# Kernel tuning notes

Hardware: AMD Instinct MI355X
Metric: run time of the kernel (lower is better)

## Reference

```python
import jax, jax.numpy as jnp
import numpy as np

IMG = 1024.0          # image height == width
OUT = 7               # roi_size
RATIO = 2             # sampling_ratio
SCALE = 1.0 / 32.0    # spatial_scale
BBOX_W = (10.0, 10.0, 5.0, 5.0)
DWH_CLIP = float(np.log(1000.0 / 16.0))


def _bilinear(feat, ys, xs):
    """feat [C,H,W]; ys [N,P,1], xs [N,1,P] -> [C,N,P,P] (torchvision semantics)."""
    C, H, W = feat.shape
    valid = (ys > -1.0) & (ys < H) & (xs > -1.0) & (xs < W)
    y = jnp.clip(ys, 0.0, H - 1.0)
    x = jnp.clip(xs, 0.0, W - 1.0)
    y0 = jnp.floor(y).astype(jnp.int32)
    x0 = jnp.floor(x).astype(jnp.int32)
    y1 = jnp.minimum(y0 + 1, H - 1)
    x1 = jnp.minimum(x0 + 1, W - 1)
    ly = y - y0
    lx = x - x0
    hy = 1.0 - ly
    hx = 1.0 - lx
    v = (feat[:, y0, x0] * (hy * hx) + feat[:, y0, x1] * (hy * lx)
         + feat[:, y1, x0] * (ly * hx) + feat[:, y1, x1] * (ly * lx))
    return jnp.where(valid, v, 0.0)


def _roi_align_image(feat, rois):
    """feat [C,H,W], rois [N,4] xyxy in image coords -> [N,C,OUT,OUT]."""
    b = rois * SCALE
    x1, y1 = b[:, 0], b[:, 1]
    rw = jnp.maximum(b[:, 2] - x1, 1.0)
    rh = jnp.maximum(b[:, 3] - y1, 1.0)
    bw = rw / OUT
    bh = rh / OUT
    # sub-bin sample offsets: [OUT*RATIO] positions along each roi edge
    g = (jnp.arange(OUT, dtype=jnp.float32)[:, None]
         + (jnp.arange(RATIO, dtype=jnp.float32)[None, :] + 0.5) / RATIO).reshape(-1)
    ys = y1[:, None] + g[None, :] * bh[:, None]   # [N, OUT*RATIO]
    xs = x1[:, None] + g[None, :] * bw[:, None]
    v = _bilinear(feat, ys[:, :, None], xs[:, None, :])          # [C,N,P,P]
    C = feat.shape[0]
    v = v.reshape(C, -1, OUT, RATIO, OUT, RATIO).mean(axis=(3, 5))  # avg over samples
    return jnp.transpose(v, (1, 0, 2, 3))


def _decode(deltas, proposals):
    """deltas [R,K*4], proposals [R,4] -> clipped boxes [R,K,4]."""
    wx, wy, ww, wh = BBOX_W
    pw = proposals[:, 2] - proposals[:, 0]
    ph = proposals[:, 3] - proposals[:, 1]
    cx = proposals[:, 0] + 0.5 * pw
    cy = proposals[:, 1] + 0.5 * ph
    d = deltas.reshape(deltas.shape[0], -1, 4)
    dx = d[..., 0] / wx
    dy = d[..., 1] / wy
    dw = jnp.minimum(d[..., 2] / ww, DWH_CLIP)
    dh = jnp.minimum(d[..., 3] / wh, DWH_CLIP)
    pcx = dx * pw[:, None] + cx[:, None]
    pcy = dy * ph[:, None] + cy[:, None]
    ppw = jnp.exp(dw) * pw[:, None]
    pph = jnp.exp(dh) * ph[:, None]
    boxes = jnp.stack([pcx - 0.5 * ppw, pcy - 0.5 * pph,
                       pcx + 0.5 * ppw, pcy + 0.5 * pph], axis=-1)
    return jnp.clip(boxes, 0.0, IMG)  # clip_boxes_to_image


def setup_inputs() -> dict:
    key = jax.random.key(0)
    ks = jax.random.split(key, 8)
    B, N, C, H, W = 2, 1024, 256, 32, 32
    feat_dim = C * OUT * OUT  # 12544
    features = jax.random.normal(ks[0], (B, C, H, W), dtype=jnp.float32)
    cxy = jax.random.uniform(ks[1], (B, N, 2), minval=0.0, maxval=IMG)
    wh = jax.random.uniform(ks[2], (B, N, 2), minval=16.0, maxval=256.0)
    p1 = jnp.clip(cxy - 0.5 * wh, 0.0, IMG)
    p2 = jnp.clip(cxy + 0.5 * wh, 0.0, IMG)
    proposals = jnp.concatenate([p1, p2], axis=-1)  # [B,N,4] valid xyxy
    w1 = jax.random.normal(ks[3], (1024, feat_dim), dtype=jnp.float32) * 0.01
    w2 = jax.random.normal(ks[4], (1024, 1024), dtype=jnp.float32) * 0.01
    wc = jax.random.normal(ks[5], (2, 1024), dtype=jnp.float32) * 0.01
    wb = jax.random.normal(ks[6], (8, 1024), dtype=jnp.float32) * 0.001
    return {"features": features, "proposals": proposals,
            "w1": w1, "b1": jnp.zeros((1024,), jnp.float32),
            "w2": w2, "b2": jnp.zeros((1024,), jnp.float32),
            "wc": wc, "bc": jnp.zeros((2,), jnp.float32),
            "wb": wb, "bb": jnp.zeros((8,), jnp.float32)}


def reference(features, proposals, w1, b1, w2, b2, wc, bc, wb, bb):
    pooled = jax.vmap(_roi_align_image)(features, proposals)   # [B,N,C,7,7]
    B, N = pooled.shape[:2]
    x = pooled.reshape(B * N, -1)                               # flatten(start_dim=1)
    x = jax.nn.relu(x @ w1.T + b1)
    x = jax.nn.relu(x @ w2.T + b2)
    cls_scores = x @ wc.T + bc                                  # [R, num_classes]
    bbox_deltas = x @ wb.T + bb                                 # [R, num_classes*4]
    pred_boxes = _decode(bbox_deltas, proposals.reshape(-1, 4)) # [R, num_classes, 4]
    pred_scores = jax.nn.softmax(cls_scores, axis=-1)
    return cls_scores, bbox_deltas, pred_boxes, pred_scores
```

## Files before the change

kernel.cpp:

```cpp
#include <hip/hip_runtime.h>
#include <hip/hip_bf16.h>
#include <stdint.h>

typedef __attribute__((ext_vector_type(8))) short bf16x8;
typedef __attribute__((ext_vector_type(4))) float f32x4;

__device__ __forceinline__ ushort f2bf(float f) {
    union { float f; uint32_t u; } c; c.f = f;
    uint32_t u = c.u;
    uint32_t r = (u + 0x7FFFu + ((u >> 16) & 1u)) >> 16;
    return (ushort)r;
}

__device__ __forceinline__ void load16_to_lds(const void* gsrc, void* ldst) {
    __builtin_amdgcn_global_load_lds(
        (const __attribute__((address_space(1))) uint32_t*)gsrc,
        (__attribute__((address_space(3))) uint32_t*)ldst,
        16, 0, 0);
}

__global__ __launch_bounds__(256) void f32_to_bf16_kernel(
    const float* __restrict__ in, ushort* __restrict__ out, int n)
{
    int i = (blockIdx.x * 256 + threadIdx.x) * 4;
    if (i >= n) return;
    float4 v = *(const float4*)(in + i);
    ushort4 o;
    o.x = f2bf(v.x); o.y = f2bf(v.y); o.z = f2bf(v.z); o.w = f2bf(v.w);
    *(ushort4*)(out + i) = o;
}

__global__ __launch_bounds__(256) void transpose_feat_kernel(
    const float* __restrict__ feat, float* __restrict__ featT)
{
    int bc = blockIdx.x;
    int b = bc >> 8;
    int c = bc & 255;
    const float* src = feat + (size_t)bc * 1024;
    float* dst = featT + (size_t)b * 262144 + c;
    #pragma unroll
    for (int i = 0; i < 4; ++i) {
        int p = i * 256 + threadIdx.x;
        dst[(size_t)p * 256] = src[p];
    }
}

__global__ __launch_bounds__(512) void roi_align_kernel(
    const float* __restrict__ featT, const float* __restrict__ props,
    ushort* __restrict__ pooled)
{
    int roi = blockIdx.x;
    int b = roi >> 10;
    __shared__ int   si0[28];
    __shared__ int   si1[28];
    __shared__ float sl[28];
    __shared__ float sv[28];
    __shared__ float Aw[7][10];
    __shared__ float Bw[7][10];
    __shared__ __align__(16) ushort outbuf[12544];
    int tid = threadIdx.x;
    if (tid < 28) {
        int axis = (tid >= 14) ? 1 : 0;
        int pp = tid - axis * 14;
        float c0 = props[roi * 4 + (axis ? 0 : 1)] * (1.f / 32.f);
        float c1 = props[roi * 4 + (axis ? 2 : 3)] * (1.f / 32.f);
        float sz = fmaxf(c1 - c0, 1.f);
        float bsz = sz * (1.f / 7.f);
        float g = (float)(pp >> 1) + ((float)(pp & 1) + 0.5f) * 0.5f;
        float c = c0 + g * bsz;
        float valid = (c > -1.f && c < 32.f) ? 1.f : 0.f;
        float cc = fminf(fmaxf(c, 0.f), 31.f);
        float fl = floorf(cc);
        int i0 = (int)fl;
        si0[tid] = i0;
        si1[tid] = min(i0 + 1, 31);
        sl[tid] = cc - fl;
        sv[tid] = valid;
    }
    __syncthreads();

    const int r0 = si0[0];
    const int c0 = si0[14];

    if (tid < 140) {
        int axis = tid / 70;
        int e = tid - axis * 70;
        int oy = e / 10, yy = e - oy * 10;
        int base = axis * 14;
        int org = axis ? c0 : r0;
        float wsum = 0.f;
        #pragma unroll
        for (int s = 0; s < 2; ++s) {
            int p = base + oy * 2 + s;
            float w = 0.f;
            if (si0[p] - org == yy) w += 1.f - sl[p];
            if (si1[p] - org == yy) w += sl[p];
            wsum += sv[p] * w;
        }
        wsum *= 0.5f;
        if (axis == 0) Aw[oy][yy] = wsum;
        else           Bw[oy][yy] = wsum;
    }
    __syncthreads();

    const int grp = tid >> 8;
    const int ch = tid & 255;
    const float* fbase = featT + (size_t)b * 262144 + ch;

    int xoff[10];
    #pragma unroll
    for (int x = 0; x < 10; ++x) xoff[x] = min(c0 + x, 31) * 256;

    if (grp == 0) {
        float t[4][10];
        #pragma unroll
        for (int oy = 0; oy < 4; ++oy)
            #pragma unroll
            for (int x = 0; x < 10; ++x) t[oy][x] = 0.f;
        #pragma unroll
        for (int y = 0; y < 10; ++y) {
            const float* frow = fbase + (size_t)min(r0 + y, 31) * 8192;
            float a0 = Aw[0][y], a1 = Aw[1][y], a2 = Aw[2][y], a3 = Aw[3][y];
            #pragma unroll
            for (int x = 0; x < 10; ++x) {
                float fv = frow[xoff[x]];
                t[0][x] += a0 * fv;
                t[1][x] += a1 * fv;
                t[2][x] += a2 * fv;
                t[3][x] += a3 * fv;
            }
        }
        #pragma unroll
        for (int oy = 0; oy < 4; ++oy)
            #pragma unroll
            for (int ox = 0; ox < 7; ++ox) {
                float o = 0.f;
                #pragma unroll
                for (int x = 0; x < 10; ++x) o += Bw[ox][x] * t[oy][x];
                outbuf[ch * 49 + oy * 7 + ox] = f2bf(o);
            }
    } else {
        float t[3][10];
        #pragma unroll
        for (int oy = 0; oy < 3; ++oy)
            #pragma unroll
            for (int x = 0; x < 10; ++x) t[oy][x] = 0.f;
        #pragma unroll
        for (int y = 0; y < 10; ++y) {
            const float* frow = fbase + (size_t)min(r0 + y, 31) * 8192;
            float a4 = Aw[4][y], a5 = Aw[5][y], a6 = Aw[6][y];
            #pragma unroll
            for (int x = 0; x < 10; ++x) {
                float fv = frow[xoff[x]];
                t[0][x] += a4 * fv;
                t[1][x] += a5 * fv;
                t[2][x] += a6 * fv;
            }
        }
        #pragma unroll
        for (int oy = 0; oy < 3; ++oy)
            #pragma unroll
            for (int ox = 0; ox < 7; ++ox) {
                float o = 0.f;
                #pragma unroll
                for (int x = 0; x < 10; ++x) o += Bw[ox][x] * t[oy][x];
                outbuf[ch * 49 + (4 + oy) * 7 + ox] = f2bf(o);
            }
    }
    __syncthreads();

    const uint4* src = (const uint4*)outbuf;
    uint4* dst = (uint4*)(pooled + (size_t)roi * 12544);
    #pragma unroll
    for (int i = 0; i < 4; ++i) {
        int idx = i * 512 + tid;
        if (idx < 1568) dst[idx] = src[idx];
    }
}

__global__ __launch_bounds__(256, 3) void gemm_bt_split(
    const ushort* __restrict__ A, const ushort* __restrict__ Bm,
    float* __restrict__ part, int M, int N, int K, int klen)
{
    constexpr int BK = 32;
    __shared__ __align__(16) ushort lA[128][BK];
    __shared__ __align__(16) ushort lB[128][BK];
    const int tid = threadIdx.x;

    const int nbx = gridDim.x, nby = gridDim.y;
    const int nwg = nbx * nby * gridDim.z;
    const int d = blockIdx.x + nbx * (blockIdx.y + nby * blockIdx.z);
    const int t = (d & 7) * (nwg >> 3) + (d >> 3);
    const int n_blk = t % nbx;
    const int m_blk = (t / nbx) % nby;
    const int k_blk = t / (nbx * nby);

    const int m0 = m_blk * 128;
    const int n0 = n_blk * 128;
    const int k_start = k_blk * klen;

    const int w = tid >> 6, l = tid & 63;
    const int wr = w >> 1, wcid = w & 1;
    const int lrow = l & 15;
    const int lkb = (((l >> 4) ^ ((lrow >> 1) & 3)) * 16);

    int sc0 = tid, sc1 = 256 + tid;
    int srow0 = sc0 >> 2, srow1 = sc1 >> 2;
    int scol0 = ((sc0 & 3) ^ ((srow0 >> 1) & 3)) * 16;
    int scol1 = ((sc1 & 3) ^ ((srow1 >> 1) & 3)) * 16;

    f32x4 acc[4][4] = {};

    for (int k0 = k_start; k0 < k_start + klen; k0 += BK) {
        __syncthreads();
        load16_to_lds((const char*)(A + (size_t)(m0 + srow0) * K + k0) + scol0, ((char*)lA) + sc0 * 16);
        load16_to_lds((const char*)(A + (size_t)(m0 + srow1) * K + k0) + scol1, ((char*)lA) + sc1 * 16);
        load16_to_lds((const char*)(Bm + (size_t)(n0 + srow0) * K + k0) + scol0, ((char*)lB) + sc0 * 16);
        load16_to_lds((const char*)(Bm + (size_t)(n0 + srow1) * K + k0) + scol1, ((char*)lB) + sc1 * 16);
        __syncthreads();

        bf16x8 af[4], bfr[4];
        #pragma unroll
        for (int m = 0; m < 4; ++m)
            af[m] = *(const bf16x8*)(((const char*)lA) + (wr * 64 + m * 16 + lrow) * 64 + lkb);
        #pragma unroll
        for (int n = 0; n < 4; ++n)
            bfr[n] = *(const bf16x8*)(((const char*)lB) + (wcid * 64 + n * 16 + lrow) * 64 + lkb);
        #pragma unroll
        for (int m = 0; m < 4; ++m)
            #pragma unroll
            for (int n = 0; n < 4; ++n)
                acc[m][n] = __builtin_amdgcn_mfma_f32_16x16x32_bf16(af[m], bfr[n], acc[m][n], 0, 0, 0);
    }

    const int r4 = (l >> 4) * 4;
    const int cc = l & 15;
    float* pb = part + (size_t)k_blk * M * N;
    #pragma unroll
    for (int m = 0; m < 4; ++m) {
        #pragma unroll
        for (int n = 0; n < 4; ++n) {
            int col = n0 + wcid * 64 + n * 16 + cc;
            #pragma unroll
            for (int j = 0; j < 4; ++j) {
                int row = m0 + wr * 64 + m * 16 + r4 + j;
                pb[(size_t)row * N + col] = acc[m][n][j];
            }
        }
    }
}

template<bool OUT_BF16>
__global__ __launch_bounds__(256) void reduce_split_kernel(
    const float* __restrict__ part, const float* __restrict__ bias,
    void* __restrict__ out, int MN, int N, int S, int relu)
{
    int i4 = (blockIdx.x * 256 + threadIdx.x) * 4;
    if (i4 >= MN) return;
    float4 a = *(const float4*)(part + i4);
    for (int s = 1; s < S; ++s) {
        float4 b = *(const float4*)(part + (size_t)s * MN + i4);
        a.x += b.x; a.y += b.y; a.z += b.z; a.w += b.w;
    }
    int bc = i4 & (N - 1);
    float4 bv = *(const float4*)(bias + bc);
    a.x += bv.x; a.y += bv.y; a.z += bv.z; a.w += bv.w;
    if (relu) {
        a.x = fmaxf(a.x, 0.f); a.y = fmaxf(a.y, 0.f);
        a.z = fmaxf(a.z, 0.f); a.w = fmaxf(a.w, 0.f);
    }
    if (OUT_BF16) {
        ushort4 o; o.x = f2bf(a.x); o.y = f2bf(a.y); o.z = f2bf(a.z); o.w = f2bf(a.w);
        *(ushort4*)((ushort*)out + i4) = o;
    } else {
        *(float4*)((float*)out + i4) = a;
    }
}

template<bool OUT_BF16>
__global__ __launch_bounds__(256) void gemm_bt(
    const ushort* __restrict__ A, const ushort* __restrict__ Bm,
    const float* __restrict__ bias, void* __restrict__ Cout,
    int M, int N, int K, int relu)
{
    constexpr int BM = 128, BN = 64, BK = 32;
    __shared__ __align__(16) ushort lA[BM][BK];
    __shared__ __align__(16) ushort lB[BN][BK];
    const int tid = threadIdx.x;
    const int m0 = blockIdx.y * BM;
    const int n0 = blockIdx.x * BN;
    const int w = tid >> 6, l = tid & 63;
    const int wr = w >> 1, wcid = w & 1;
    const int lrow = l & 15, lk = (l >> 4) * 8;

    f32x4 acc[4][2] = {};

    for (int k0 = 0; k0 < K; k0 += BK) {
        __syncthreads();
        #pragma unroll
        for (int i = 0; i < 2; ++i) {
            int chunk = i * 256 + tid;
            int row = chunk >> 2;
            int colb = (chunk & 3) * 16;
            load16_to_lds((const char*)(A + (size_t)(m0 + row) * K + k0) + colb, ((char*)lA) + chunk * 16);
        }
        {
            int chunk = tid;
            int row = chunk >> 2;
            int colb = (chunk & 3) * 16;
            load16_to_lds((const char*)(Bm + (size_t)(n0 + row) * K + k0) + colb, ((char*)lB) + chunk * 16);
        }
        __syncthreads();

        bf16x8 af[4], bfr[2];
        #pragma unroll
        for (int m = 0; m < 4; ++m)
            af[m] = *(const bf16x8*)&lA[wr * 64 + m * 16 + lrow][lk];
        #pragma unroll
        for (int n = 0; n < 2; ++n)
            bfr[n] = *(const bf16x8*)&lB[wcid * 32 + n * 16 + lrow][lk];
        #pragma unroll
        for (int m = 0; m < 4; ++m)
            #pragma unroll
            for (int n = 0; n < 2; ++n)
                acc[m][n] = __builtin_amdgcn_mfma_f32_16x16x32_bf16(af[m], bfr[n], acc[m][n], 0, 0, 0);
    }

    const int r4 = (l >> 4) * 4;
    const int cc = l & 15;
    #pragma unroll
    for (int m = 0; m < 4; ++m) {
        #pragma unroll
        for (int n = 0; n < 2; ++n) {
            int col = n0 + wcid * 32 + n * 16 + cc;
            float bv = bias[col];
            #pragma unroll
            for (int j = 0; j < 4; ++j) {
                int row = m0 + wr * 64 + m * 16 + r4 + j;
                float v = acc[m][n][j] + bv;
                if (relu) v = fmaxf(v, 0.f);
                if (OUT_BF16) ((ushort*)Cout)[(size_t)row * N + col] = f2bf(v);
                else          ((float*)Cout)[(size_t)row * N + col] = v;
            }
        }
    }
}

__global__ __launch_bounds__(256) void heads_kernel(
    const float* __restrict__ x2,
    const float* __restrict__ wc, const float* __restrict__ bc,
    const float* __restrict__ wb, const float* __restrict__ bb,
    float* __restrict__ out)
{
    int w = threadIdx.x >> 6, l = threadIdx.x & 63;
    int row = blockIdx.x * 4 + w;
    const float* xr = x2 + (size_t)row * 1024;
    float acc[10];
    #pragma unroll
    for (int o = 0; o < 10; ++o) acc[o] = 0.f;
    for (int i = 0; i < 16; ++i) {
        int k = i * 64 + l;
        float xv = xr[k];
        #pragma unroll
        for (int o = 0; o < 2; ++o) acc[o] += xv * wc[o * 1024 + k];
        #pragma unroll
        for (int o = 0; o < 8; ++o) acc[2 + o] += xv * wb[o * 1024 + k];
    }
    #pragma unroll
    for (int o = 0; o < 10; ++o) {
        float v = acc[o];
        #pragma unroll
        for (int s = 32; s > 0; s >>= 1) v += __shfl_xor(v, s, 64);
        acc[o] = v;
    }
    if (l == 0) {
        float* cls = out;
        float* bbx = out + 2048 * 2;
        cls[row * 2 + 0] = acc[0] + bc[0];
        cls[row * 2 + 1] = acc[1] + bc[1];
        #pragma unroll
        for (int o = 0; o < 8; ++o) bbx[row * 8 + o] = acc[2 + o] + bb[o];
    }
}

__global__ __launch_bounds__(256) void decode_kernel(
    const float* __restrict__ props, float* __restrict__ out)
{
    int r = blockIdx.x * 256 + threadIdx.x;
    if (r >= 2048) return;
    const float* cls = out;
    const float* bbx = out + 4096;
    float* boxes  = out + 20480;
    float* scores = out + 36864;
    float px1 = props[r * 4 + 0], py1 = props[r * 4 + 1];
    float px2 = props[r * 4 + 2], py2 = props[r * 4 + 3];
    float pw = px2 - px1, ph = py2 - py1;
    float cx = px1 + 0.5f * pw, cy = py1 + 0.5f * ph;
    const float CLIP = 4.135166556742356f;
    #pragma unroll
    for (int k = 0; k < 2; ++k) {
        float dx = bbx[r * 8 + k * 4 + 0] * 0.1f;
        float dy = bbx[r * 8 + k * 4 + 1] * 0.1f;
        float dw = fminf(bbx[r * 8 + k * 4 + 2] * 0.2f, CLIP);
        float dh = fminf(bbx[r * 8 + k * 4 + 3] * 0.2f, CLIP);
        float pcx = dx * pw + cx, pcy = dy * ph + cy;
        float ppw = expf(dw) * pw, pph = expf(dh) * ph;
        float v0 = pcx - 0.5f * ppw, v1 = pcy - 0.5f * pph;
        float v2 = pcx + 0.5f * ppw, v3 = pcy + 0.5f * pph;
        boxes[r * 8 + k * 4 + 0] = fminf(fmaxf(v0, 0.f), 1024.f);
        boxes[r * 8 + k * 4 + 1] = fminf(fmaxf(v1, 0.f), 1024.f);
        boxes[r * 8 + k * 4 + 2] = fminf(fmaxf(v2, 0.f), 1024.f);
        boxes[r * 8 + k * 4 + 3] = fminf(fmaxf(v3, 0.f), 1024.f);
    }
    float s0 = cls[r * 2], s1 = cls[r * 2 + 1];
    float m = fmaxf(s0, s1);
    float e0 = expf(s0 - m), e1 = expf(s1 - m);
    float inv = 1.f / (e0 + e1);
    scores[r * 2 + 0] = e0 * inv;
    scores[r * 2 + 1] = e1 * inv;
}

extern "C" void kernel_launch(void* const* d_in, const int* in_sizes, int n_in,
                              void* d_out, int out_size, void* d_ws, size_t ws_size,
                              hipStream_t stream) {
    const float* feat  = (const float*)d_in[0];
    const float* props = (const float*)d_in[1];
    const float* w1    = (const float*)d_in[2];
    const float* b1    = (const float*)d_in[3];
    const float* w2    = (const float*)d_in[4];
    const float* b2    = (const float*)d_in[5];
    const float* wc    = (const float*)d_in[6];
    const float* bc    = (const float*)d_in[7];
    const float* wb    = (const float*)d_in[8];
    const float* bb    = (const float*)d_in[9];
    float* out = (float*)d_out;

    char* ws = (char*)d_ws;
    ushort* pooled = (ushort*)(ws);
    ushort* w1b    = (ushort*)(ws + 51380224);
    ushort* w2b    = (ushort*)(ws + 51380224 + 25690112);
    ushort* x1     = (ushort*)(ws + 79167488);
    float*  x2     = (float*) (ws + 83361792);
    float*  featT  = (float*) (ws + 83361792);
    float*  part   = (float*) (ws + 91750400);
    const size_t WS_NEED = 91750400 + 33554432;

    const int M = 2048, N = 1024;
    const int MN = M * N;

    f32_to_bf16_kernel<<<12845056 / 1024, 256, 0, stream>>>(w1, w1b, 12845056);
    f32_to_bf16_kernel<<<1048576 / 1024, 256, 0, stream>>>(w2, w2b, 1048576);
    transpose_feat_kernel<<<512, 256, 0, stream>>>(feat, featT);
    roi_align_kernel<<<2048, 512, 0, stream>>>(featT, props, pooled);

    if (ws_size >= WS_NEED) {
        gemm_bt_split<<<dim3(N / 128, M / 128, 4), 256, 0, stream>>>(pooled, w1b, part, M, N, 12544, 3136);
        reduce_split_kernel<true ><<<MN / 1024, 256, 0, stream>>>(part, b1, x1, MN, N, 4, 1);
        gemm_bt_split<<<dim3(N / 128, M / 128, 4), 256, 0, stream>>>(x1, w2b, part, M, N, 1024, 256);
        reduce_split_kernel<false><<<MN / 1024, 256, 0, stream>>>(part, b2, x2, MN, N, 4, 1);
    } else {
        gemm_bt<true ><<<dim3(N / 64, M / 128), 256, 0, stream>>>(pooled, w1b, b1, x1, M, N, 12544, 1);
        gemm_bt<false><<<dim3(N / 64, M / 128), 256, 0, stream>>>(x1, w2b, b2, x2, M, N, 1024, 1);
    }

    heads_kernel<<<512, 256, 0, stream>>>(x2, wc, bc, wb, bb, out);
    decode_kernel<<<8, 256, 0, stream>>>(props, out);
}
```

Measured before the change: 190.5 us.

## Double-buffer LDS in split-K GEMM and raise first GEMM split to 8

```diff
diff --git a/kernel.cpp b/kernel.cpp
--- a/kernel.cpp
+++ b/kernel.cpp
@@ -178,13 +178,13 @@
     }
 }
 
-__global__ __launch_bounds__(256, 3) void gemm_bt_split(
+__global__ __launch_bounds__(256) void gemm_bt_split(
     const ushort* __restrict__ A, const ushort* __restrict__ Bm,
     float* __restrict__ part, int M, int N, int K, int klen)
 {
     constexpr int BK = 32;
-    __shared__ __align__(16) ushort lA[128][BK];
-    __shared__ __align__(16) ushort lB[128][BK];
+    __shared__ __align__(16) ushort lA[2][128][BK];
+    __shared__ __align__(16) ushort lB[2][128][BK];
     const int tid = threadIdx.x;
 
     const int nbx = gridDim.x, nby = gridDim.y;
@@ -204,33 +204,50 @@
     const int lrow = l & 15;
     const int lkb = (((l >> 4) ^ ((lrow >> 1) & 3)) * 16);
 
-    int sc0 = tid, sc1 = 256 + tid;
-    int srow0 = sc0 >> 2, srow1 = sc1 >> 2;
-    int scol0 = ((sc0 & 3) ^ ((srow0 >> 1) & 3)) * 16;
-    int scol1 = ((sc1 & 3) ^ ((srow1 >> 1) & 3)) * 16;
+    const int sc0 = tid, sc1 = 256 + tid;
+    const int srow0 = sc0 >> 2, srow1 = sc1 >> 2;
+    const int scol0 = ((sc0 & 3) ^ ((srow0 >> 1) & 3)) * 16;
+    const int scol1 = ((sc1 & 3) ^ ((srow1 >> 1) & 3)) * 16;
+
+    const int nsteps = klen / BK;
+
+    {
+        int k0 = k_start;
+        load16_to_lds((const char*)(A + (size_t)(m0 + srow0) * K + k0) + scol0, ((char*)lA[0]) + sc0 * 16);
+        load16_to_lds((const char*)(A + (size_t)(m0 + srow1) * K + k0) + scol1, ((char*)lA[0]) + sc1 * 16);
+        load16_to_lds((const char*)(Bm + (size_t)(n0 + srow0) * K + k0) + scol0, ((char*)lB[0]) + sc0 * 16);
+        load16_to_lds((const char*)(Bm + (size_t)(n0 + srow1) * K + k0) + scol1, ((char*)lB[0]) + sc1 * 16);
+    }
+    __syncthreads();
 
     f32x4 acc[4][4] = {};
-
-    for (int k0 = k_start; k0 < k_start + klen; k0 += BK) {
-        __syncthreads();
-        load16_to_lds((const char*)(A + (size_t)(m0 + srow0) * K + k0) + scol0, ((char*)lA) + sc0 * 16);
-        load16_to_lds((const char*)(A + (size_t)(m0 + srow1) * K + k0) + scol1, ((char*)lA) + sc1 * 16);
-        load16_to_lds((const char*)(Bm + (size_t)(n0 + srow0) * K + k0) + scol0, ((char*)lB) + sc0 * 16);
-        load16_to_lds((const char*)(Bm + (size_t)(n0 + srow1) * K + k0) + scol1, ((char*)lB) + sc1 * 16);
-        __syncthreads();
+    int cur = 0;
+
+    for (int ts = 0; ts < nsteps; ++ts) {
+        if (ts + 1 < nsteps) {
+            int k0 = k_start + (ts + 1) * BK;
+            int nxt = cur ^ 1;
+            load16_to_lds((const char*)(A + (size_t)(m0 + srow0) * K + k0) + scol0, ((char*)lA[nxt]) + sc0 * 16);
+            load16_to_lds((const char*)(A + (size_t)(m0 + srow1) * K + k0) + scol1, ((char*)lA[nxt]) + sc1 * 16);
+            load16_to_lds((const char*)(Bm + (size_t)(n0 + srow0) * K + k0) + scol0, ((char*)lB[nxt]) + sc0 * 16);
+            load16_to_lds((const char*)(Bm + (size_t)(n0 + srow1) * K + k0) + scol1, ((char*)lB[nxt]) + sc1 * 16);
+        }
 
         bf16x8 af[4], bfr[4];
         #pragma unroll
         for (int m = 0; m < 4; ++m)
-            af[m] = *(const bf16x8*)(((const char*)lA) + (wr * 64 + m * 16 + lrow) * 64 + lkb);
+            af[m] = *(const bf16x8*)(((const char*)lA[cur]) + (wr * 64 + m * 16 + lrow) * 64 + lkb);
         #pragma unroll
         for (int n = 0; n < 4; ++n)
-            bfr[n] = *(const bf16x8*)(((const char*)lB) + (wcid * 64 + n * 16 + lrow) * 64 + lkb);
+            bfr[n] = *(const bf16x8*)(((const char*)lB[cur]) + (wcid * 64 + n * 16 + lrow) * 64 + lkb);
         #pragma unroll
         for (int m = 0; m < 4; ++m)
             #pragma unroll
             for (int n = 0; n < 4; ++n)
                 acc[m][n] = __builtin_amdgcn_mfma_f32_16x16x32_bf16(af[m], bfr[n], acc[m][n], 0, 0, 0);
+
+        __syncthreads();
+        cur ^= 1;
     }
 
     const int r4 = (l >> 4) * 4;
@@ -443,7 +460,8 @@
     float*  x2     = (float*) (ws + 83361792);
     float*  featT  = (float*) (ws + 83361792);
     float*  part   = (float*) (ws + 91750400);
-    const size_t WS_NEED = 91750400 + 33554432;
+    const size_t WS_NEED4 = 91750400 + 33554432;
+    const size_t WS_NEED8 = 91750400 + 67108864;
 
     const int M = 2048, N = 1024;
     const int MN = M * N;
@@ -453,7 +471,12 @@
     transpose_feat_kernel<<<512, 256, 0, stream>>>(feat, featT);
     roi_align_kernel<<<2048, 512, 0, stream>>>(featT, props, pooled);
 
-    if (ws_size >= WS_NEED) {
+    if (ws_size >= WS_NEED8) {
+        gemm_bt_split<<<dim3(N / 128, M / 128, 8), 256, 0, stream>>>(pooled, w1b, part, M, N, 12544, 1568);
+        reduce_split_kernel<true ><<<MN / 1024, 256, 0, stream>>>(part, b1, x1, MN, N, 8, 1);
+        gemm_bt_split<<<dim3(N / 128, M / 128, 4), 256, 0, stream>>>(x1, w2b, part, M, N, 1024, 256);
+        reduce_split_kernel<false><<<MN / 1024, 256, 0, stream>>>(part, b2, x2, MN, N, 4, 1);
+    } else if (ws_size >= WS_NEED4) {
         gemm_bt_split<<<dim3(N / 128, M / 128, 4), 256, 0, stream>>>(pooled, w1b, part, M, N, 12544, 3136);
         reduce_split_kernel<true ><<<MN / 1024, 256, 0, stream>>>(part, b1, x1, MN, N, 4, 1);
         gemm_bt_split<<<dim3(N / 128, M / 128, 4), 256, 0, stream>>>(x1, w2b, part, M, N, 1024, 256);
```

New measurement: 185.6 us. 1.03x faster.
